# Performance work log

Measured on AMD Instinct MI355X. Metric: run time of the kernel, lower is better.

Reference implementation:

```python
import jax, jax.numpy as jnp
import numpy as np

TEMP_UPDATE = 1e-05
EPS = 1e-12  # torch F.normalize eps


def _l2norm(x, axis):
    n = jnp.sqrt(jnp.sum(x * x, axis=axis, keepdims=True))
    return x / jnp.maximum(n, EPS)


def setup_inputs() -> dict:
    key = jax.random.key(0)
    k1, k2 = jax.random.split(key)
    query = jax.random.normal(k1, (64, 256, 512), dtype=jnp.float32)
    keys = jax.random.normal(k2, (2048, 512), dtype=jnp.float32)
    return {"query": query, "keys": keys}


def reference(query, keys):
    bs, t, d = query.shape
    m = keys.shape[0]
    # F.normalize(query, dim=2)
    q = _l2norm(query, axis=2)
    qr = q.reshape(bs * t, d)                      # [N, d]
    score = qr @ keys.T                            # [N, m]
    score_query = jax.nn.softmax(score, axis=0)    # softmax over queries per slot
    score_memory = jax.nn.softmax(score, axis=1)   # softmax over slots per query
    # topk(1) over memory dim -> argmax slot per query
    g = jnp.argmax(score_memory, axis=1)           # [N] int
    col_max = jnp.max(score_query, axis=0)         # [m]
    # weight per query: score_query[n, g_n] / max(score_query[:, g_n])
    w = jnp.take_along_axis(score_query, g[:, None], axis=1)[:, 0] / col_max[g]
    # fused scatter-add replacing the per-slot python loop
    query_update = jax.ops.segment_sum(w[:, None] * qr, g, num_segments=m)  # [m, d]
    updated = _l2norm(TEMP_UPDATE * query_update + keys, axis=1)
    return jax.lax.stop_gradient(updated)  # original returns .detach()
```

## Files before the change

kernel.cpp:

```cpp
#include <hip/hip_runtime.h>
#include <math.h>

#define N_Q     16384
#define DDIM    512
#define M_SLOTS 2048
#define EPSN    1e-12f
#define TEMPU   1e-5f
#define KSCALE  25.4f
#define QSCALE  127.0f
#define INV_S   (1.0f / (127.0f * 25.4f))
#define NZBLK   72

typedef unsigned int u32;
typedef unsigned long long u64;
typedef __attribute__((ext_vector_type(4))) int i32x4;

__device__ __forceinline__ void gld_lds16(const void* g, void* l) {
    __builtin_amdgcn_global_load_lds(
        (const __attribute__((address_space(1))) u32*)(g),
        (__attribute__((address_space(3))) u32*)(l), 16, 0, 0);
}
__device__ __forceinline__ float block_reduce_sum_128(float v, float* sred, int t) {
    #pragma unroll
    for (int o = 32; o > 0; o >>= 1) v += __shfl_down(v, o, 64);
    if ((t & 63) == 0) sred[t >> 6] = v;
    __syncthreads();
    return sred[0] + sred[1];
}
__device__ __forceinline__ char q8(float x, float s) {
    int v = __float2int_rn(x * s);
    v = v < -127 ? -127 : (v > 127 ? 127 : v);
    return (char)v;
}

__global__ __launch_bounds__(128) void k_prep(const float* __restrict__ q,
                                              const float* __restrict__ keys,
                                              char* __restrict__ qi8,
                                              char* __restrict__ ki8,
                                              float4* __restrict__ zbase) {
    __shared__ float sred[2];
    int b = blockIdx.x;
    int t = threadIdx.x;
    if (b < N_Q) {
        float4 v = ((const float4*)(q + (size_t)b * DDIM))[t];
        float ss = v.x * v.x + v.y * v.y + v.z * v.z + v.w * v.w;
        ss = block_reduce_sum_128(ss, sred, t);
        float s = QSCALE / fmaxf(sqrtf(ss), EPSN);
        char4 o;
        o.x = q8(v.x, s);
        o.y = q8(v.y, s);
        o.z = q8(v.z, s);
        o.w = q8(v.w, s);
        ((char4*)(qi8 + (size_t)b * DDIM))[t] = o;
    } else if (b < N_Q + M_SLOTS) {
        int r = b - N_Q;
        float4 v = ((const float4*)(keys + (size_t)r * DDIM))[t];
        char4 o;
        o.x = q8(v.x, KSCALE);
        o.y = q8(v.y, KSCALE);
        o.z = q8(v.z, KSCALE);
        o.w = q8(v.w, KSCALE);
        ((char4*)(ki8 + (size_t)r * DDIM))[t] = o;
    } else {
        int idx = (b - (N_Q + M_SLOTS)) * 128 + t;
        zbase[idx] = make_float4(0.f, 0.f, 0.f, 0.f);
    }
}

__global__ __launch_bounds__(256) void k_score(const char* __restrict__ qi8,
                                               const char* __restrict__ ki8,
                                               u64* __restrict__ rowpack,
                                               u32* __restrict__ colmax) {
    __shared__ char sA[3][128 * 64];
    __shared__ char sB[3][128 * 64];

    int t = threadIdx.x;
    int lane = t & 63;
    int wid = t >> 6;
    int wrow = wid >> 1;
    int wcol = wid & 1;
    int lr = lane & 15;
    int kc = lane >> 4;

    int n0 = blockIdx.y * 128;
    int j0 = blockIdx.x * 128;

    int srow = t >> 2;
    int scolB = 16 * ((t & 3) ^ ((t >> 3) & 3));

    const char* gA0 = qi8 + (size_t)(n0 + srow) * DDIM + scolB;
    const char* gA1 = qi8 + (size_t)(n0 + 64 + srow) * DDIM + scolB;
    const char* gB0 = ki8 + (size_t)(j0 + srow) * DDIM + scolB;
    const char* gB1 = ki8 + (size_t)(j0 + 64 + srow) * DDIM + scolB;

    int rsw = 16 * ((t >> 1) & 3);
    (void)rsw;

    i32x4 acc[4][4] = {};

#define STAGE(buf, k0)  do {                                   \
        gld_lds16(gA0 + (k0), &sA[buf][t * 16]);               \
        gld_lds16(gA1 + (k0), &sA[buf][4096 + t * 16]);        \
        gld_lds16(gB0 + (k0), &sB[buf][t * 16]);               \
        gld_lds16(gB1 + (k0), &sB[buf][4096 + t * 16]);        \
    } while (0)

    STAGE(0, 0);
    STAGE(1, 64);
    asm volatile("s_waitcnt vmcnt(4)" ::: "memory");
    __builtin_amdgcn_s_barrier();
    __builtin_amdgcn_sched_barrier(0);

    const int rchunk = 16 * 0;
    (void)rchunk;

    #pragma unroll
    for (int kt = 0; kt < 8; ++kt) {
        const int cur = kt % 3;
        if (kt < 6) STAGE((kt + 2) % 3, (kt + 2) * 64);

        i32x4 a[4], b[4];
        int roff = 16 * (kc ^ ((lr >> 1) & 3));
        #pragma unroll
        for (int i = 0; i < 4; ++i)
            a[i] = *(const i32x4*)&sA[cur][(wrow * 64 + i * 16 + lr) * 64 + roff];
        #pragma unroll
        for (int j = 0; j < 4; ++j)
            b[j] = *(const i32x4*)&sB[cur][(wcol * 64 + j * 16 + lr) * 64 + roff];
        __builtin_amdgcn_s_setprio(1);
        #pragma unroll
        for (int i = 0; i < 4; ++i)
            #pragma unroll
            for (int j = 0; j < 4; ++j)
                acc[i][j] = __builtin_amdgcn_mfma_i32_16x16x64_i8(a[i], b[j], acc[i][j], 0, 0, 0);
        __builtin_amdgcn_s_setprio(0);

        if (kt < 6)       asm volatile("s_waitcnt vmcnt(4)" ::: "memory");
        else if (kt == 6) asm volatile("s_waitcnt vmcnt(0)" ::: "memory");
        if (kt < 7) {
            __builtin_amdgcn_s_barrier();
            __builtin_amdgcn_sched_barrier(0);
        }
    }
#undef STAGE

    #pragma unroll
    for (int i = 0; i < 4; ++i) {
        #pragma unroll
        for (int r = 0; r < 4; ++r) {
            int v = acc[i][0][r];
            int c = j0 + wcol * 64 + lr;
            #pragma unroll
            for (int j = 1; j < 4; ++j) {
                int vj = acc[i][j][r];
                int cj = j0 + wcol * 64 + j * 16 + lr;
                if (vj > v) { v = vj; c = cj; }
            }
            #pragma unroll
            for (int off = 1; off < 16; off <<= 1) {
                int ov = __shfl_xor(v, off, 64);
                int oc = __shfl_xor(c, off, 64);
                if (ov > v || (ov == v && oc < c)) { v = ov; c = oc; }
            }
            if (lr == 0) {
                int grow = n0 + wrow * 64 + i * 16 + kc * 4 + r;
                u64 pk = ((u64)(u32)(v ^ 0x80000000) << 32) | (u64)(~(u32)c);
                atomicMax(rowpack + grow, pk);
            }
        }
    }
    #pragma unroll
    for (int j = 0; j < 4; ++j) {
        int m = acc[0][j][0];
        #pragma unroll
        for (int i = 0; i < 4; ++i)
            #pragma unroll
            for (int r = 0; r < 4; ++r) m = max(m, acc[i][j][r]);
        m = max(m, __shfl_xor(m, 16, 64));
        m = max(m, __shfl_xor(m, 32, 64));
        if (kc == 0) atomicMax(colmax + j0 + wcol * 64 + j * 16 + lr,
                               (u32)m ^ 0x80000000u);
    }
}

__global__ __launch_bounds__(256) void k_hist(const u64* __restrict__ rowpack,
                                              u32* __restrict__ cnt) {
    int n = blockIdx.x * 256 + threadIdx.x;
    u64 p = rowpack[n];
    int g = (int)(~(u32)(p & 0xFFFFFFFFull));
    atomicAdd(cnt + g, 1u);
}

__global__ __launch_bounds__(256) void k_scan(const u32* __restrict__ cnt,
                                              u32* __restrict__ start,
                                              u32* __restrict__ cursor) {
    __shared__ u32 wsum[4];
    int t = threadIdx.x;
    int lane = t & 63, w = t >> 6;
    u32 local[8], s = 0;
    #pragma unroll
    for (int i = 0; i < 8; ++i) { local[i] = cnt[t * 8 + i]; s += local[i]; }
    u32 x = s;
    #pragma unroll
    for (int off = 1; off < 64; off <<= 1) {
        u32 y = __shfl_up(x, off, 64);
        if (lane >= off) x += y;
    }
    if (lane == 63) wsum[w] = x;
    __syncthreads();
    u32 base = 0;
    #pragma unroll
    for (int i = 0; i < 4; ++i) if (i < w) base += wsum[i];
    u32 run = base + x - s;
    #pragma unroll
    for (int i = 0; i < 8; ++i) {
        start[t * 8 + i] = run;
        cursor[t * 8 + i] = run;
        run += local[i];
    }
}

__global__ __launch_bounds__(256) void k_fill(const u64* __restrict__ rowpack,
                                              const u32* __restrict__ colmax,
                                              u32* __restrict__ cursor,
                                              u32* __restrict__ perm,
                                              float* __restrict__ wval) {
    int n = blockIdx.x * 256 + threadIdx.x;
    u64 p = rowpack[n];
    int vi = (int)(((u32)(p >> 32)) ^ 0x80000000u);
    int g = (int)(~(u32)(p & 0xFFFFFFFFull));
    int cm = (int)(colmax[g] ^ 0x80000000u);
    float w = expf((float)(vi - cm) * INV_S);
    u32 pos = atomicAdd(cursor + g, 1u);
    perm[pos] = (u32)n;
    wval[pos] = w;
}

__global__ __launch_bounds__(128) void k_gather_final(const char* __restrict__ qi8,
                                                      const u32* __restrict__ start,
                                                      const u32* __restrict__ cnt,
                                                      const u32* __restrict__ perm,
                                                      const float* __restrict__ wval,
                                                      const float* __restrict__ keys,
                                                      float* __restrict__ out) {
    __shared__ float sred[2];
    int j = blockIdx.x;
    int t = threadIdx.x;
    u32 s = start[j];
    u32 e = s + cnt[j];
    float ax = 0.f, ay = 0.f, az = 0.f, aw = 0.f;
    for (u32 i = s; i < e; ++i) {
        u32 n = perm[i];
        float wq = wval[i] * (1.0f / 127.0f);
        char4 q4 = ((const char4*)(qi8 + (size_t)n * DDIM))[t];
        ax = fmaf(wq, (float)q4.x, ax);
        ay = fmaf(wq, (float)q4.y, ay);
        az = fmaf(wq, (float)q4.z, az);
        aw = fmaf(wq, (float)q4.w, aw);
    }
    float4 k4 = ((const float4*)(keys + (size_t)j * DDIM))[t];
    float4 v;
    v.x = fmaf(TEMPU, ax, k4.x);
    v.y = fmaf(TEMPU, ay, k4.y);
    v.z = fmaf(TEMPU, az, k4.z);
    v.w = fmaf(TEMPU, aw, k4.w);
    float ss = v.x * v.x + v.y * v.y + v.z * v.z + v.w * v.w;
    ss = block_reduce_sum_128(ss, sred, t);
    float inv = 1.0f / fmaxf(sqrtf(ss), EPSN);
    v.x *= inv; v.y *= inv; v.z *= inv; v.w *= inv;
    ((float4*)(out + (size_t)j * DDIM))[t] = v;
}

extern "C" void kernel_launch(void* const* d_in, const int* in_sizes, int n_in,
                              void* d_out, int out_size, void* d_ws, size_t ws_size,
                              hipStream_t stream) {
    const float* query = (const float*)d_in[0];
    const float* keys  = (const float*)d_in[1];
    float* out = (float*)d_out;

    char* ws = (char*)d_ws;
    const size_t OFF_QI8   = 0;
    const size_t OFF_ROW   = 8388608;
    const size_t OFF_CMAX  = OFF_ROW + 131072;
    const size_t OFF_CNT   = OFF_CMAX + 8192;
    const size_t OFF_START = OFF_CNT + 8192;
    const size_t OFF_CUR   = OFF_START + 8192;
    const size_t OFF_PERM  = OFF_CUR + 8192;
    const size_t OFF_W     = OFF_PERM + 65536;
    const size_t OFF_KI8   = OFF_W + 65536;

    char*   qi8    = ws + OFF_QI8;
    u64*    rowpack= (u64*)(ws + OFF_ROW);
    u32*    cmax   = (u32*)(ws + OFF_CMAX);
    u32*    cnt    = (u32*)(ws + OFF_CNT);
    u32*    start  = (u32*)(ws + OFF_START);
    u32*    cursor = (u32*)(ws + OFF_CUR);
    u32*    perm   = (u32*)(ws + OFF_PERM);
    float*  wval   = (float*)(ws + OFF_W);
    char*   ki8    = ws + OFF_KI8;

    k_prep<<<N_Q + M_SLOTS + NZBLK, 128, 0, stream>>>(query, keys, qi8, ki8,
                                                      (float4*)(ws + OFF_ROW));

    dim3 g2(M_SLOTS / 128, N_Q / 128);
    k_score<<<g2, 256, 0, stream>>>(qi8, ki8, rowpack, cmax);

    k_hist<<<N_Q / 256, 256, 0, stream>>>(rowpack, cnt);
    k_scan<<<1, 256, 0, stream>>>(cnt, start, cursor);
    k_fill<<<N_Q / 256, 256, 0, stream>>>(rowpack, cmax, cursor, perm, wval);
    k_gather_final<<<M_SLOTS, 128, 0, stream>>>(qi8, start, cnt, perm, wval, keys, out);
}
```

Before: 84.88 us.

## Replace histogram/scan bucketing with fixed-capacity buckets plus overflow list

```diff
diff --git a/kernel.cpp b/kernel.cpp
--- a/kernel.cpp
+++ b/kernel.cpp
@@ -9,7 +9,8 @@
 #define KSCALE  25.4f
 #define QSCALE  127.0f
 #define INV_S   (1.0f / (127.0f * 25.4f))
-#define NZBLK   72
+#define NZBLK   73
+#define BCAP    32
 
 typedef unsigned int u32;
 typedef unsigned long long u64;
@@ -86,15 +87,12 @@
     int j0 = blockIdx.x * 128;
 
     int srow = t >> 2;
-    int scolB = 16 * ((t & 3) ^ ((t >> 3) & 3));
+    int scolB = (t & 3) * 16;
 
     const char* gA0 = qi8 + (size_t)(n0 + srow) * DDIM + scolB;
     const char* gA1 = qi8 + (size_t)(n0 + 64 + srow) * DDIM + scolB;
     const char* gB0 = ki8 + (size_t)(j0 + srow) * DDIM + scolB;
     const char* gB1 = ki8 + (size_t)(j0 + 64 + srow) * DDIM + scolB;
-
-    int rsw = 16 * ((t >> 1) & 3);
-    (void)rsw;
 
     i32x4 acc[4][4] = {};
 
@@ -111,29 +109,23 @@
     __builtin_amdgcn_s_barrier();
     __builtin_amdgcn_sched_barrier(0);
 
-    const int rchunk = 16 * 0;
-    (void)rchunk;
-
     #pragma unroll
     for (int kt = 0; kt < 8; ++kt) {
         const int cur = kt % 3;
         if (kt < 6) STAGE((kt + 2) % 3, (kt + 2) * 64);
 
         i32x4 a[4], b[4];
-        int roff = 16 * (kc ^ ((lr >> 1) & 3));
         #pragma unroll
         for (int i = 0; i < 4; ++i)
-            a[i] = *(const i32x4*)&sA[cur][(wrow * 64 + i * 16 + lr) * 64 + roff];
+            a[i] = *(const i32x4*)&sA[cur][(wrow * 64 + i * 16 + lr) * 64 + kc * 16];
         #pragma unroll
         for (int j = 0; j < 4; ++j)
-            b[j] = *(const i32x4*)&sB[cur][(wcol * 64 + j * 16 + lr) * 64 + roff];
-        __builtin_amdgcn_s_setprio(1);
+            b[j] = *(const i32x4*)&sB[cur][(wcol * 64 + j * 16 + lr) * 64 + kc * 16];
         #pragma unroll
         for (int i = 0; i < 4; ++i)
             #pragma unroll
             for (int j = 0; j < 4; ++j)
                 acc[i][j] = __builtin_amdgcn_mfma_i32_16x16x64_i8(a[i], b[j], acc[i][j], 0, 0, 0);
-        __builtin_amdgcn_s_setprio(0);
 
         if (kt < 6)       asm volatile("s_waitcnt vmcnt(4)" ::: "memory");
         else if (kt == 6) asm volatile("s_waitcnt vmcnt(0)" ::: "memory");
@@ -183,80 +175,69 @@
     }
 }
 
-__global__ __launch_bounds__(256) void k_hist(const u64* __restrict__ rowpack,
-                                              u32* __restrict__ cnt) {
-    int n = blockIdx.x * 256 + threadIdx.x;
-    u64 p = rowpack[n];
-    int g = (int)(~(u32)(p & 0xFFFFFFFFull));
-    atomicAdd(cnt + g, 1u);
-}
-
-__global__ __launch_bounds__(256) void k_scan(const u32* __restrict__ cnt,
-                                              u32* __restrict__ start,
-                                              u32* __restrict__ cursor) {
-    __shared__ u32 wsum[4];
-    int t = threadIdx.x;
-    int lane = t & 63, w = t >> 6;
-    u32 local[8], s = 0;
-    #pragma unroll
-    for (int i = 0; i < 8; ++i) { local[i] = cnt[t * 8 + i]; s += local[i]; }
-    u32 x = s;
-    #pragma unroll
-    for (int off = 1; off < 64; off <<= 1) {
-        u32 y = __shfl_up(x, off, 64);
-        if (lane >= off) x += y;
-    }
-    if (lane == 63) wsum[w] = x;
-    __syncthreads();
-    u32 base = 0;
-    #pragma unroll
-    for (int i = 0; i < 4; ++i) if (i < w) base += wsum[i];
-    u32 run = base + x - s;
-    #pragma unroll
-    for (int i = 0; i < 8; ++i) {
-        start[t * 8 + i] = run;
-        cursor[t * 8 + i] = run;
-        run += local[i];
-    }
-}
-
 __global__ __launch_bounds__(256) void k_fill(const u64* __restrict__ rowpack,
                                               const u32* __restrict__ colmax,
-                                              u32* __restrict__ cursor,
-                                              u32* __restrict__ perm,
-                                              float* __restrict__ wval) {
+                                              u32* __restrict__ cur,
+                                              u32* __restrict__ bperm,
+                                              float* __restrict__ bw,
+                                              u32* __restrict__ ovf_cnt,
+                                              u32* __restrict__ ovf_n,
+                                              float* __restrict__ ovf_w) {
     int n = blockIdx.x * 256 + threadIdx.x;
     u64 p = rowpack[n];
     int vi = (int)(((u32)(p >> 32)) ^ 0x80000000u);
     int g = (int)(~(u32)(p & 0xFFFFFFFFull));
     int cm = (int)(colmax[g] ^ 0x80000000u);
     float w = expf((float)(vi - cm) * INV_S);
-    u32 pos = atomicAdd(cursor + g, 1u);
-    perm[pos] = (u32)n;
-    wval[pos] = w;
+    u32 pos = atomicAdd(cur + g, 1u);
+    if (pos < BCAP) {
+        bperm[g * BCAP + pos] = (u32)n;
+        bw[g * BCAP + pos] = w;
+    } else {
+        u32 o = atomicAdd(ovf_cnt, 1u);
+        ovf_n[o] = ((u32)g << 16) | (u32)n;
+        ovf_w[o] = w;
+    }
 }
 
 __global__ __launch_bounds__(128) void k_gather_final(const char* __restrict__ qi8,
-                                                      const u32* __restrict__ start,
-                                                      const u32* __restrict__ cnt,
-                                                      const u32* __restrict__ perm,
-                                                      const float* __restrict__ wval,
+                                                      const u32* __restrict__ cur,
+                                                      const u32* __restrict__ bperm,
+                                                      const float* __restrict__ bw,
+                                                      const u32* __restrict__ ovf_cnt,
+                                                      const u32* __restrict__ ovf_n,
+                                                      const float* __restrict__ ovf_w,
                                                       const float* __restrict__ keys,
                                                       float* __restrict__ out) {
     __shared__ float sred[2];
     int j = blockIdx.x;
     int t = threadIdx.x;
-    u32 s = start[j];
-    u32 e = s + cnt[j];
+    u32 c = cur[j];
+    u32 cnt = c < BCAP ? c : BCAP;
     float ax = 0.f, ay = 0.f, az = 0.f, aw = 0.f;
-    for (u32 i = s; i < e; ++i) {
-        u32 n = perm[i];
-        float wq = wval[i] * (1.0f / 127.0f);
+    for (u32 i = 0; i < cnt; ++i) {
+        u32 n = bperm[j * BCAP + i];
+        float wq = bw[j * BCAP + i] * (1.0f / 127.0f);
         char4 q4 = ((const char4*)(qi8 + (size_t)n * DDIM))[t];
         ax = fmaf(wq, (float)q4.x, ax);
         ay = fmaf(wq, (float)q4.y, ay);
         az = fmaf(wq, (float)q4.z, az);
         aw = fmaf(wq, (float)q4.w, aw);
+    }
+    if (c > BCAP) {
+        u32 oc = *ovf_cnt;
+        for (u32 i = 0; i < oc; ++i) {
+            u32 e = ovf_n[i];
+            if ((e >> 16) == (u32)j) {
+                u32 n = e & 0xFFFFu;
+                float wq = ovf_w[i] * (1.0f / 127.0f);
+                char4 q4 = ((const char4*)(qi8 + (size_t)n * DDIM))[t];
+                ax = fmaf(wq, (float)q4.x, ax);
+                ay = fmaf(wq, (float)q4.y, ay);
+                az = fmaf(wq, (float)q4.z, az);
+                aw = fmaf(wq, (float)q4.w, aw);
+            }
+        }
     }
     float4 k4 = ((const float4*)(keys + (size_t)j * DDIM))[t];
     float4 v;
@@ -282,21 +263,23 @@
     const size_t OFF_QI8   = 0;
     const size_t OFF_ROW   = 8388608;
     const size_t OFF_CMAX  = OFF_ROW + 131072;
-    const size_t OFF_CNT   = OFF_CMAX + 8192;
-    const size_t OFF_START = OFF_CNT + 8192;
-    const size_t OFF_CUR   = OFF_START + 8192;
-    const size_t OFF_PERM  = OFF_CUR + 8192;
-    const size_t OFF_W     = OFF_PERM + 65536;
-    const size_t OFF_KI8   = OFF_W + 65536;
+    const size_t OFF_CUR   = OFF_CMAX + 8192;
+    const size_t OFF_OVFC  = OFF_CUR + 8192;
+    const size_t OFF_BPERM = OFF_OVFC + 2048;
+    const size_t OFF_BW    = OFF_BPERM + 262144;
+    const size_t OFF_OVFN  = OFF_BW + 262144;
+    const size_t OFF_OVFW  = OFF_OVFN + 65536;
+    const size_t OFF_KI8   = OFF_OVFW + 65536;
 
     char*   qi8    = ws + OFF_QI8;
     u64*    rowpack= (u64*)(ws + OFF_ROW);
     u32*    cmax   = (u32*)(ws + OFF_CMAX);
-    u32*    cnt    = (u32*)(ws + OFF_CNT);
-    u32*    start  = (u32*)(ws + OFF_START);
-    u32*    cursor = (u32*)(ws + OFF_CUR);
-    u32*    perm   = (u32*)(ws + OFF_PERM);
-    float*  wval   = (float*)(ws + OFF_W);
+    u32*    cur    = (u32*)(ws + OFF_CUR);
+    u32*    ovfc   = (u32*)(ws + OFF_OVFC);
+    u32*    bperm  = (u32*)(ws + OFF_BPERM);
+    float*  bw     = (float*)(ws + OFF_BW);
+    u32*    ovfn   = (u32*)(ws + OFF_OVFN);
+    float*  ovfw   = (float*)(ws + OFF_OVFW);
     char*   ki8    = ws + OFF_KI8;
 
     k_prep<<<N_Q + M_SLOTS + NZBLK, 128, 0, stream>>>(query, keys, qi8, ki8,
@@ -305,8 +288,8 @@
     dim3 g2(M_SLOTS / 128, N_Q / 128);
     k_score<<<g2, 256, 0, stream>>>(qi8, ki8, rowpack, cmax);
 
-    k_hist<<<N_Q / 256, 256, 0, stream>>>(rowpack, cnt);
-    k_scan<<<1, 256, 0, stream>>>(cnt, start, cursor);
-    k_fill<<<N_Q / 256, 256, 0, stream>>>(rowpack, cmax, cursor, perm, wval);
-    k_gather_final<<<M_SLOTS, 128, 0, stream>>>(qi8, start, cnt, perm, wval, keys, out);
-}
+    k_fill<<<N_Q / 256, 256, 0, stream>>>(rowpack, cmax, cur, bperm, bw,
+                                          ovfc, ovfn, ovfw);
+    k_gather_final<<<M_SLOTS, 128, 0, stream>>>(qi8, cur, bperm, bw,
+                                                ovfc, ovfn, ovfw, keys, out);
+}
```

Result: faster. 72.19 us (-15.0%).
